# Performance work log

Hardware: AMD Instinct MI355X
Metric: run time of the kernel (lower is better)

## Reference

```python
import jax, jax.numpy as jnp
import numpy as np

B, S, D, H, DK, DFF = 4, 1024, 1024, 16, 64, 4096
EPS = 1e-5


def _layernorm(x, w, b):
    mu = jnp.mean(x, axis=-1, keepdims=True)
    var = jnp.mean((x - mu) ** 2, axis=-1, keepdims=True)
    return (x - mu) / jnp.sqrt(var + EPS) * w + b


def setup_inputs() -> dict:
    root = jax.random.key(0)
    ks = jax.random.split(root, 16)
    g = lambda k, shape, s=0.02: (jax.random.normal(k, shape, dtype=jnp.float32) * s)
    return {
        "mask": 1,
        "query": jax.random.normal(ks[0], (B, S, D), dtype=jnp.float32),
        "key": jax.random.normal(ks[1], (B, S, D), dtype=jnp.float32),
        "values": jax.random.normal(ks[2], (B, S, D), dtype=jnp.float32),
        "Wq": g(ks[3], (D, D)), "bq": jnp.zeros((D,), jnp.float32),
        "Wk": g(ks[4], (D, D)), "bk": jnp.zeros((D,), jnp.float32),
        "Wv": g(ks[5], (D, D)), "bv": jnp.zeros((D,), jnp.float32),
        "Wo": g(ks[6], (D, D)), "bo": jnp.zeros((D,), jnp.float32),
        "gammas": g(ks[7], (H, 1, 1), 0.5),
        "ln1_w": jnp.ones((D,), jnp.float32), "ln1_b": jnp.zeros((D,), jnp.float32),
        "W1": g(ks[8], (DFF, D)), "b1": jnp.zeros((DFF,), jnp.float32),
        "W2": g(ks[9], (D, DFF)), "b2": jnp.zeros((D,), jnp.float32),
        "ln2_w": jnp.ones((D,), jnp.float32), "ln2_b": jnp.zeros((D,), jnp.float32),
    }


def _forward(mask, query, key, values, Wq, bq, Wk, bk, Wv, bv, Wo, bo, gammas,
             ln1_w, ln1_b, W1, b1, W2, b2, ln2_w, ln2_b):
    # mask is a static Python int (the triu offset)
    allowed = jnp.triu(jnp.ones((S, S), dtype=jnp.float32), k=mask) == 0  # [S,S] bool

    def proj(x, W, b):  # [B,S,D] -> [B,H,S,DK]
        return (x @ W.T + b).reshape(B, S, H, DK).transpose(0, 2, 1, 3)

    q = proj(query, Wq, bq)
    k = proj(key, Wk, bk)
    v = proj(values, Wv, bv)

    scores = jnp.einsum('bhid,bhjd->bhij', q, k) / jnp.sqrt(jnp.float32(DK))

    # distance-decay factor, computed without gradient (torch.no_grad + detach)
    def dist_block(sc):
        sc_ = jax.nn.softmax(sc, axis=-1) * allowed.astype(sc.dtype)
        distcum = jnp.cumsum(sc_, axis=-1)
        disttot = jnp.sum(sc_, axis=-1, keepdims=True)
        idx = jnp.arange(S, dtype=jnp.float32)
        pos = jnp.abs(idx[None, :] - idx[:, None])[None, None]  # [1,1,S,S]
        return jnp.sqrt(jnp.clip((disttot - distcum) * pos, 0.0, None))
    dist_scores = jax.lax.stop_gradient(dist_block(scores))

    gamma = -jax.nn.softplus(gammas)[None]  # [1,H,1,1]
    total_effect = jnp.clip(jnp.exp(dist_scores * gamma), 1e-5, 1e5)
    scores = scores * total_effect
    scores = jnp.where(allowed, scores, jnp.float32(-1e20))
    attn = jax.nn.softmax(scores, axis=-1)
    if mask == 0:  # zero_pad first query row
        attn = attn.at[:, :, 0, :].set(0.0)

    out = jnp.einsum('bhij,bhjd->bhid', attn, v)
    concat = out.transpose(0, 2, 1, 3).reshape(B, S, D)
    attn_out = concat @ Wo.T + bo

    x = _layernorm(query + attn_out, ln1_w, ln1_b)
    ffn = jax.nn.relu(x @ W1.T + b1) @ W2.T + b2
    return _layernorm(x + ffn, ln2_w, ln2_b)


def reference(mask, query, key, values, Wq, bq, Wk, bk, Wv, bv, Wo, bo, gammas,
              ln1_w, ln1_b, W1, b1, W2, b2, ln2_w, ln2_b):
    return _forward(mask, query, key, values, Wq, bq, Wk, bk, Wv, bv, Wo, bo,
                    gammas, ln1_w, ln1_b, W1, b1, W2, b2, ln2_w, ln2_b)
```

## Files before the change

### kernel.cpp

```cpp
#include <hip/hip_runtime.h>
#include <hip/hip_bf16.h>
#include <math.h>

#define BB   4
#define SS   1024
#define DDIM 1024
#define HH   16
#define DKK  64
#define DFFF 4096
#define JC2  64

typedef __attribute__((ext_vector_type(8))) short short8;
typedef __attribute__((ext_vector_type(4))) float f32x4;
typedef unsigned short ushort;

__device__ __forceinline__ ushort f2bf(float f) {
    unsigned int u = __float_as_uint(f);
    unsigned int r = (u + 0x7FFFu + ((u >> 16) & 1u)) >> 16;
    return (ushort)r;
}
__device__ __forceinline__ short8 pack8(float4 f0, float4 f1) {
    short8 s;
    s[0] = (short)f2bf(f0.x); s[1] = (short)f2bf(f0.y);
    s[2] = (short)f2bf(f0.z); s[3] = (short)f2bf(f0.w);
    s[4] = (short)f2bf(f1.x); s[5] = (short)f2bf(f1.y);
    s[6] = (short)f2bf(f1.z); s[7] = (short)f2bf(f1.w);
    return s;
}

#define GLD16(g, l) __builtin_amdgcn_global_load_lds( \
    (const __attribute__((address_space(1))) unsigned int*)(g), \
    (__attribute__((address_space(3))) unsigned int*)(l), 16, 0, 0)

__device__ __forceinline__ float fexp2(float x) { return __builtin_amdgcn_exp2f(x); }

__device__ __forceinline__ float scan16(float x) {
    x += __int_as_float(__builtin_amdgcn_update_dpp(0, __float_as_int(x), 0x111, 0xF, 0xF, true));
    x += __int_as_float(__builtin_amdgcn_update_dpp(0, __float_as_int(x), 0x112, 0xF, 0xF, true));
    x += __int_as_float(__builtin_amdgcn_update_dpp(0, __float_as_int(x), 0x114, 0xF, 0xF, true));
    x += __int_as_float(__builtin_amdgcn_update_dpp(0, __float_as_int(x), 0x118, 0xF, 0xF, true));
    return x;
}
__device__ __forceinline__ float bcast15(float x) {
    return __int_as_float(__builtin_amdgcn_ds_swizzle(__float_as_int(x), 0x1F0));
}

__device__ __forceinline__ float block_reduce_sum(float v, float* red, int tid) {
#pragma unroll
    for (int off = 32; off; off >>= 1) v += __shfl_xor(v, off);
    __syncthreads();
    if ((tid & 63) == 0) red[tid >> 6] = v;
    __syncthreads();
    return red[0] + red[1] + red[2] + red[3];
}

struct CvtArgs { const float* s[9]; ushort* d[9]; unsigned int n[9]; };
__global__ __launch_bounds__(256) void convert_bf(CvtArgs a) {
    const int seg = blockIdx.y;
    size_t idx = ((size_t)blockIdx.x * 256 + threadIdx.x) * 8;
    if (idx >= a.n[seg]) return;
    const float* s = a.s[seg];
    float4 f0 = *(const float4*)(s + idx);
    float4 f1 = *(const float4*)(s + idx + 4);
    *(short8*)(a.d[seg] + idx) = pack8(f0, f1);
}

template <int BM, typename TC, bool RELU>
__device__ __forceinline__ void gemm_core(const ushort* __restrict__ A,
                                          const ushort* __restrict__ Bm,
                                          const float* __restrict__ bias,
                                          TC* __restrict__ C,
                                          int M, int N, int K,
                                          int bm, int bn) {
    constexpr int MT = BM / 32;
    constexpr int PA = BM / 32;
    __shared__ ushort A_s[BM * 64];
    __shared__ ushort B_s[128 * 64];
    const int t = threadIdx.x;
    const int lane = t & 63, w = t >> 6;
    const int wr = w >> 1, wc = w & 1;
    const int fm = lane & 15, fq = lane >> 4;
    const int srl = lane >> 3;
    const int sg8 = ((lane & 7) ^ srl) << 3;

    f32x4 acc[MT][4];
#pragma unroll
    for (int mt = 0; mt < MT; mt++)
#pragma unroll
        for (int nt = 0; nt < 4; nt++) acc[mt][nt] = (f32x4){0.f, 0.f, 0.f, 0.f};

    for (int kt = 0; kt < K; kt += 64) {
        __syncthreads();
#pragma unroll
        for (int p = 0; p < PA; ++p) {
            int rowg = (w * PA + p) * 8;
            GLD16(A + (size_t)(bm + rowg + srl) * K + kt + sg8, &A_s[rowg * 64]);
        }
#pragma unroll
        for (int p = 0; p < 4; ++p) {
            int rowg = (w * 4 + p) * 8;
            GLD16(Bm + (size_t)(bn + rowg + srl) * K + kt + sg8, &B_s[rowg * 64]);
        }
        __syncthreads();

        short8 av[2][MT], bv[2][4];
        const int sw = fm & 7;
#pragma unroll
        for (int mt = 0; mt < MT; ++mt) {
            int row = wr * (BM / 2) + mt * 16 + fm;
#pragma unroll
            for (int ks = 0; ks < 2; ++ks)
                av[ks][mt] = *(const short8*)&A_s[row * 64 + (((ks * 4 + fq) ^ sw) << 3)];
        }
#pragma unroll
        for (int nt = 0; nt < 4; ++nt) {
            int row = wc * 64 + nt * 16 + fm;
#pragma unroll
            for (int ks = 0; ks < 2; ++ks)
                bv[ks][nt] = *(const short8*)&B_s[row * 64 + (((ks * 4 + fq) ^ sw) << 3)];
        }
#pragma unroll
        for (int ks = 0; ks < 2; ++ks)
#pragma unroll
            for (int mt = 0; mt < MT; ++mt)
#pragma unroll
                for (int nt = 0; nt < 4; ++nt)
                    acc[mt][nt] = __builtin_amdgcn_mfma_f32_16x16x32_bf16(
                        av[ks][mt], bv[ks][nt], acc[mt][nt], 0, 0, 0);
    }

#pragma unroll
    for (int mt = 0; mt < MT; mt++) {
        int row0 = bm + wr * (BM / 2) + mt * 16 + fq * 4;
#pragma unroll
        for (int nt = 0; nt < 4; nt++) {
            int col = bn + wc * 64 + nt * 16 + fm;
            float bsv = bias[col];
#pragma unroll
            for (int r = 0; r < 4; r++) {
                float val = acc[mt][nt][r] + bsv;
                if (RELU) val = fmaxf(val, 0.f);
                if constexpr (sizeof(TC) == 4)
                    ((float*)C)[(size_t)(row0 + r) * N + col] = val;
                else
                    ((ushort*)C)[(size_t)(row0 + r) * N + col] = f2bf(val);
            }
        }
    }
}

template <int BM, typename TC, bool RELU>
__global__ __launch_bounds__(256, 2) void gemm_bf(const ushort* __restrict__ A,
                                                  const ushort* __restrict__ Bm,
                                                  const float* __restrict__ bias,
                                                  TC* __restrict__ C,
                                                  int M, int N, int K) {
    gemm_core<BM, TC, RELU>(A, Bm, bias, C, M, N, K,
                            blockIdx.y * BM, blockIdx.x * 128);
}

struct QkvArgs { const ushort* A[3]; const ushort* B[3]; const float* bias[3]; ushort* C[3]; };
__global__ __launch_bounds__(256, 2) void gemm_qkv(QkvArgs qa) {
    const int g = blockIdx.z;
    gemm_core<128, ushort, false>(qa.A[g], qa.B[g], qa.bias[g], qa.C[g],
                                  BB * SS, DDIM, DDIM,
                                  blockIdx.y * 128, blockIdx.x * 128);
}

__global__ __launch_bounds__(256, 4) void attn_flash(
    const ushort* __restrict__ Q, const ushort* __restrict__ Kg,
    const ushort* __restrict__ Vg, const float* __restrict__ gammas,
    const int* __restrict__ maskp, ushort* __restrict__ out) {
    __shared__ short QP[64 * 72];
    __shared__ short Ks[JC2 * 72];
    __shared__ short Vts[64 * 72];

    const int t = threadIdx.x;
    const int lane = t & 63, w = t >> 6;
    const int col = lane & 15;
    const int quad = lane >> 4;

    const int bid = blockIdx.x;
    const int it = bid >> 6;
    const int bh = bid & 63;
    const int h = bh & (HH - 1);
    const int b = bh >> 4;
    const int i0 = it * 64;
    const int mask = *maskp;

    const float LOG2E = 1.44269504f;
    const float SC2 = 0.125f * LOG2E;
    const float g0 = gammas[h];
    const float gnat = -((g0 > 20.f) ? g0 : log1pf(__expf(g0)));
    const float g2 = gnat * LOG2E;

    const size_t qbase = ((size_t)(b * SS + i0)) * DDIM + h * DKK;
    const size_t kvbase = ((size_t)b * SS) * DDIM + h * DKK;

    {
        int r = t >> 2, d0 = (t & 3) << 4;
        const ushort* gq = Q + qbase + (size_t)r * DDIM + d0;
        *(short8*)&QP[r * 72 + d0]     = *(const short8*)(gq);
        *(short8*)&QP[r * 72 + d0 + 8] = *(const short8*)(gq + 8);
    }
    __syncthreads();
    const short8 qa0 = *(const short8*)&QP[(w * 16 + col) * 72 + quad * 8];
    const short8 qa1 = *(const short8*)&QP[(w * 16 + col) * 72 + 32 + quad * 8];

    float m1[4], su[4], smT[4], gi4[4];
    int lim4[4];
#pragma unroll
    for (int r = 0; r < 4; ++r) {
        m1[r] = -3.4e38f; su[r] = 0.f; smT[r] = 0.f;
        int gi = i0 + w * 16 + quad * 4 + r;
        gi4[r] = (float)gi;
        lim4[r] = gi + mask;
    }

    for (int ck = 0; ck < SS / JC2; ++ck) {
        const int jc = ck * JC2;
        __syncthreads();
        {
            int j = t >> 2, d0 = (t & 3) << 4;
            const ushort* gk = Kg + kvbase + (size_t)(jc + j) * DDIM + d0;
            *(short8*)&Ks[j * 72 + d0]     = *(const short8*)(gk);
            *(short8*)&Ks[j * 72 + d0 + 8] = *(const short8*)(gk + 8);
        }
        __syncthreads();
#pragma unroll
        for (int g = 0; g < 4; ++g) {
            short8 kb0 = *(const short8*)&Ks[(g * 16 + col) * 72 + quad * 8];
            short8 kb1 = *(const short8*)&Ks[(g * 16 + col) * 72 + 32 + quad * 8];
            f32x4 c = (f32x4){0.f, 0.f, 0.f, 0.f};
            c = __builtin_amdgcn_mfma_f32_16x16x32_bf16(qa0, kb0, c, 0, 0, 0);
            c = __builtin_amdgcn_mfma_f32_16x16x32_bf16(qa1, kb1, c, 0, 0, 0);
            int j = jc + g * 16 + col;
#pragma unroll
            for (int r = 0; r < 4; ++r) {
                float s2 = c[r] * SC2;
                m1[r] = fmaxf(m1[r], s2);
                float ev = fexp2(s2);
                su[r] += ev;
                smT[r] += (j < lim4[r]) ? ev : 0.f;
            }
        }
    }
#pragma unroll
    for (int off = 1; off < 16; off <<= 1) {
#pragma unroll
        for (int r = 0; r < 4; ++r) {
            m1[r] = fmaxf(m1[r], __shfl_xor(m1[r], off, 16));
            su[r] += __shfl_xor(su[r], off, 16);
            smT[r] += __shfl_xor(smT[r], off, 16);
        }
    }
    float lse2[4], smTn[4], ms2[4];
#pragma unroll
    for (int r = 0; r < 4; ++r) {
        lse2[r] = __log2f(su[r]);
        smTn[r] = smT[r] / su[r];
        ms2[r]  = fmaxf(m1[r], 0.f);
    }

    const int nck2 = min(SS / JC2, max(1, (i0 + 62 + mask) / 64 + 1));

    float l2[4], carry[4];
    f32x4 o[4];
#pragma unroll
    for (int r = 0; r < 4; ++r) { l2[r] = 0.f; carry[r] = 0.f; }
#pragma unroll
    for (int dg = 0; dg < 4; ++dg) o[dg] = (f32x4){0.f, 0.f, 0.f, 0.f};

    short* Pw = &QP[w * 16 * 72];

    for (int ck = 0; ck < nck2; ++ck) {
        const int jc = ck * JC2;
        __syncthreads();
        {
            int j = t >> 2, d0 = (t & 3) << 4;
            const ushort* gk = Kg + kvbase + (size_t)(jc + j) * DDIM + d0;
            *(short8*)&Ks[j * 72 + d0]     = *(const short8*)(gk);
            *(short8*)&Ks[j * 72 + d0 + 8] = *(const short8*)(gk + 8);
        }
        {
            int j = t & 63, dq = t >> 6, d0 = dq * 16;
            const ushort* gv = Vg + kvbase + (size_t)(jc + j) * DDIM + d0;
            short8 v0 = *(const short8*)(gv);
            short8 v1 = *(const short8*)(gv + 8);
#pragma unroll
            for (int k = 0; k < 8; ++k) {
                Vts[(d0 + k) * 72 + j]     = v0[k];
                Vts[(d0 + 8 + k) * 72 + j] = v1[k];
            }
        }
        __syncthreads();

#pragma unroll
        for (int g = 0; g < 4; ++g) {
            short8 kb0 = *(const short8*)&Ks[(g * 16 + col) * 72 + quad * 8];
            short8 kb1 = *(const short8*)&Ks[(g * 16 + col) * 72 + 32 + quad * 8];
            f32x4 c = (f32x4){0.f, 0.f, 0.f, 0.f};
            c = __builtin_amdgcn_mfma_f32_16x16x32_bf16(qa0, kb0, c, 0, 0, 0);
            c = __builtin_amdgcn_mfma_f32_16x16x32_bf16(qa1, kb1, c, 0, 0, 0);
            const int j = jc + g * 16 + col;
            const float jf = (float)j;
#pragma unroll
            for (int r = 0; r < 4; ++r) {
                float s2 = c[r] * SC2;
                float pj = fexp2(s2 - lse2[r]);
                float incl = (j < lim4[r]) ? pj : 0.f;
                incl = scan16(incl);
                float tot = bcast15(incl);
                float Cc = carry[r] + incl;
                carry[r] += tot;
                float pos = fabsf(jf - gi4[r]);
                float d2 = fmaxf((smTn[r] - Cc) * pos, 0.f);
                float dist = __builtin_amdgcn_sqrtf(d2);
                float eff = fmaxf(fexp2(g2 * dist), 1e-5f);
                float pe = fexp2(s2 * eff - ms2[r]);
                float p = (j < lim4[r]) ? pe : 0.f;
                l2[r] += p;
                Pw[(quad * 4 + r) * 72 + g * 16 + col] = (short)f2bf(p);
            }
        }
        __syncthreads();
#pragma unroll
        for (int kg = 0; kg < 2; ++kg) {
            short8 pa = *(const short8*)&Pw[col * 72 + kg * 32 + quad * 8];
#pragma unroll
            for (int dg = 0; dg < 4; ++dg) {
                short8 vb = *(const short8*)&Vts[(dg * 16 + col) * 72 + kg * 32 + quad * 8];
                o[dg] = __builtin_amdgcn_mfma_f32_16x16x32_bf16(pa, vb, o[dg], 0, 0, 0);
            }
        }
    }

#pragma unroll
    for (int off = 1; off < 16; off <<= 1)
#pragma unroll
        for (int r = 0; r < 4; ++r) l2[r] += __shfl_xor(l2[r], off, 16);

#pragma unroll
    for (int r = 0; r < 4; ++r) {
        int irow = i0 + w * 16 + quad * 4 + r;
        float scl = 1.f / l2[r];
        if (mask == 0 && irow == 0) scl = 0.f;
        size_t base = ((size_t)(b * SS) + irow) * DDIM + h * DKK;
#pragma unroll
        for (int dg = 0; dg < 4; ++dg)
            out[base + dg * 16 + col] = f2bf(o[dg][r] * scl);
    }
}

template <bool WB>
__global__ __launch_bounds__(256) void add_ln(const float* __restrict__ R,
                                              const float* __restrict__ Y,
                                              const float* __restrict__ w,
                                              const float* __restrict__ bb,
                                              float* __restrict__ out,
                                              ushort* __restrict__ obf) {
    const int row = blockIdx.x;
    const int tid = threadIdx.x;
    __shared__ float red[4];
    __shared__ float xs[DDIM];
    const size_t base = (size_t)row * DDIM;
    float s = 0.f, s2 = 0.f;
#pragma unroll
    for (int l = 0; l < 4; l++) {
        int idx = tid + l * 256;
        float x = R[base + idx] + Y[base + idx];
        xs[idx] = x;
        s += x;
        s2 += x * x;
    }
    s = block_reduce_sum(s, red, tid);
    s2 = block_reduce_sum(s2, red, tid);
    const float mu = s * (1.f / DDIM);
    const float var = s2 * (1.f / DDIM) - mu * mu;
    const float rstd = rsqrtf(var + 1e-5f);
#pragma unroll
    for (int l = 0; l < 4; l++) {
        int idx = tid + l * 256;
        float v = (xs[idx] - mu) * rstd * w[idx] + bb[idx];
        out[base + idx] = v;
        if (WB) obf[base + idx] = f2bf(v);
    }
}

extern "C" void kernel_launch(void* const* d_in, const int* in_sizes, int n_in,
                              void* d_out, int out_size, void* d_ws, size_t ws_size,
                              hipStream_t stream) {
    const int*   maskp  = (const int*)d_in[0];
    const float* query  = (const float*)d_in[1];
    const float* key    = (const float*)d_in[2];
    const float* values = (const float*)d_in[3];
    const float* Wq = (const float*)d_in[4];
    const float* bq = (const float*)d_in[5];
    const float* Wk = (const float*)d_in[6];
    const float* bk = (const float*)d_in[7];
    const float* Wv = (const float*)d_in[8];
    const float* bv = (const float*)d_in[9];
    const float* Wo = (const float*)d_in[10];
    const float* bo = (const float*)d_in[11];
    const float* gammas = (const float*)d_in[12];
    const float* ln1w = (const float*)d_in[13];
    const float* ln1b = (const float*)d_in[14];
    const float* W1 = (const float*)d_in[15];
    const float* b1 = (const float*)d_in[16];
    const float* W2 = (const float*)d_in[17];
    const float* b2 = (const float*)d_in[18];
    const float* ln2w = (const float*)d_in[19];
    const float* ln2b = (const float*)d_in[20];

    const int M = BB * SS;
    const size_t MB = 1048576;
    char* wsb = (char*)d_ws;
    ushort* Wq_bf = (ushort*)(wsb + 0 * MB);
    ushort* Wk_bf = (ushort*)(wsb + 8 * MB);
    ushort* Wv_bf = (ushort*)(wsb + 16 * MB);
    ushort* Wo_bf = (ushort*)(wsb + 24 * MB);
    ushort* W1_bf = (ushort*)(wsb + 32 * MB);
    ushort* W2_bf = (ushort*)(wsb + 40 * MB);
    ushort* qi_bf = (ushort*)(wsb + 48 * MB);
    ushort* ki_bf = (ushort*)(wsb + 56 * MB);
    ushort* vi_bf = (ushort*)(wsb + 64 * MB);
    ushort* Qb    = (ushort*)(wsb + 72 * MB);
    ushort* Kb    = (ushort*)(wsb + 80 * MB);
    ushort* Vb    = (ushort*)(wsb + 88 * MB);
    ushort* ATTb  = (ushort*)(wsb + 96 * MB);
    float*  Yf    = (float*)(wsb + 104 * MB);
    float*  xf    = (float*)(wsb + 48 * MB);
    ushort* x_bf  = (ushort*)(wsb + 64 * MB);
    ushort* hidden= (ushort*)(wsb + 72 * MB);

    dim3 blk(256);

    const unsigned int N4M = 4u * 1024 * 1024, N1M = 1024 * 1024;
    CvtArgs ca;
    ca.s[0] = query; ca.s[1] = key; ca.s[2] = values;
    ca.s[3] = Wq; ca.s[4] = Wk; ca.s[5] = Wv; ca.s[6] = Wo;
    ca.s[7] = W1; ca.s[8] = W2;
    ca.d[0] = qi_bf; ca.d[1] = ki_bf; ca.d[2] = vi_bf;
    ca.d[3] = Wq_bf; ca.d[4] = Wk_bf; ca.d[5] = Wv_bf; ca.d[6] = Wo_bf;
    ca.d[7] = W1_bf; ca.d[8] = W2_bf;
    ca.n[0] = N4M; ca.n[1] = N4M; ca.n[2] = N4M;
    ca.n[3] = N1M; ca.n[4] = N1M; ca.n[5] = N1M; ca.n[6] = N1M;
    ca.n[7] = N4M; ca.n[8] = N4M;
    convert_bf<<<dim3(2048, 9), blk, 0, stream>>>(ca);

    QkvArgs qa;
    qa.A[0] = qi_bf; qa.A[1] = ki_bf; qa.A[2] = vi_bf;
    qa.B[0] = Wq_bf; qa.B[1] = Wk_bf; qa.B[2] = Wv_bf;
    qa.bias[0] = bq; qa.bias[1] = bk; qa.bias[2] = bv;
    qa.C[0] = Qb; qa.C[1] = Kb; qa.C[2] = Vb;
    gemm_qkv<<<dim3(8, 32, 3), blk, 0, stream>>>(qa);

    attn_flash<<<dim3(BB * HH * 16), blk, 0, stream>>>(Qb, Kb, Vb, gammas, maskp, ATTb);

    gemm_bf<64, float, false><<<dim3(8, 64), blk, 0, stream>>>(ATTb, Wo_bf, bo, Yf, M, DDIM, DDIM);

    add_ln<true><<<dim3(M), blk, 0, stream>>>(query, Yf, ln1w, ln1b, xf, x_bf);

    gemm_bf<128, ushort, true><<<dim3(32, 32), blk, 0, stream>>>(x_bf, W1_bf, b1, hidden, M, DFFF, DDIM);

    gemm_bf<64, float, false><<<dim3(8, 64), blk, 0, stream>>>(hidden, W2_bf, b2, Yf, M, DDIM, DFFF);

    add_ln<false><<<dim3(M), blk, 0, stream>>>(xf, Yf, ln2w, ln2b, (float*)d_out, nullptr);
}
```

Baseline: 418.0 us.

## Split-K the output and FFN2 GEMMs with 128-row tiles, reduce in LayerNorm

```diff
diff --git a/kernel.cpp b/kernel.cpp
--- a/kernel.cpp
+++ b/kernel.cpp
@@ -65,12 +65,11 @@
     *(short8*)(a.d[seg] + idx) = pack8(f0, f1);
 }
 
-template <int BM, typename TC, bool RELU>
-__device__ __forceinline__ void gemm_core(const ushort* __restrict__ A,
-                                          const ushort* __restrict__ Bm,
+template <int BM, typename TC, bool RELU, bool BIAS>
+__device__ __forceinline__ void gemm_core(const ushort* __restrict__ A, int lda,
+                                          const ushort* __restrict__ Bm, int ldb,
                                           const float* __restrict__ bias,
-                                          TC* __restrict__ C,
-                                          int M, int N, int K,
+                                          TC* __restrict__ C, int N, int Klen,
                                           int bm, int bn) {
     constexpr int MT = BM / 32;
     constexpr int PA = BM / 32;
@@ -89,17 +88,17 @@
 #pragma unroll
         for (int nt = 0; nt < 4; nt++) acc[mt][nt] = (f32x4){0.f, 0.f, 0.f, 0.f};
 
-    for (int kt = 0; kt < K; kt += 64) {
+    for (int kt = 0; kt < Klen; kt += 64) {
         __syncthreads();
 #pragma unroll
         for (int p = 0; p < PA; ++p) {
             int rowg = (w * PA + p) * 8;
-            GLD16(A + (size_t)(bm + rowg + srl) * K + kt + sg8, &A_s[rowg * 64]);
+            GLD16(A + (size_t)(bm + rowg + srl) * lda + kt + sg8, &A_s[rowg * 64]);
         }
 #pragma unroll
         for (int p = 0; p < 4; ++p) {
             int rowg = (w * 4 + p) * 8;
-            GLD16(Bm + (size_t)(bn + rowg + srl) * K + kt + sg8, &B_s[rowg * 64]);
+            GLD16(Bm + (size_t)(bn + rowg + srl) * ldb + kt + sg8, &B_s[rowg * 64]);
         }
         __syncthreads();
 
@@ -135,7 +134,7 @@
 #pragma unroll
         for (int nt = 0; nt < 4; nt++) {
             int col = bn + wc * 64 + nt * 16 + fm;
-            float bsv = bias[col];
+            float bsv = BIAS ? bias[col] : 0.f;
 #pragma unroll
             for (int r = 0; r < 4; r++) {
                 float val = acc[mt][nt][r] + bsv;
@@ -154,17 +153,27 @@
                                                   const ushort* __restrict__ Bm,
                                                   const float* __restrict__ bias,
                                                   TC* __restrict__ C,
-                                                  int M, int N, int K) {
-    gemm_core<BM, TC, RELU>(A, Bm, bias, C, M, N, K,
-                            blockIdx.y * BM, blockIdx.x * 128);
+                                                  int N, int K) {
+    gemm_core<BM, TC, RELU, true>(A, K, Bm, K, bias, C, N, K,
+                                  blockIdx.y * BM, blockIdx.x * 128);
 }
 
 struct QkvArgs { const ushort* A[3]; const ushort* B[3]; const float* bias[3]; ushort* C[3]; };
 __global__ __launch_bounds__(256, 2) void gemm_qkv(QkvArgs qa) {
     const int g = blockIdx.z;
-    gemm_core<128, ushort, false>(qa.A[g], qa.B[g], qa.bias[g], qa.C[g],
-                                  BB * SS, DDIM, DDIM,
-                                  blockIdx.y * 128, blockIdx.x * 128);
+    gemm_core<128, ushort, false, true>(qa.A[g], DDIM, qa.B[g], DDIM,
+                                        qa.bias[g], qa.C[g], DDIM, DDIM,
+                                        blockIdx.y * 128, blockIdx.x * 128);
+}
+
+struct SkArgs { const ushort* A; const ushort* Bm; float* C0; float* C1; int lda; int Klen; };
+__global__ __launch_bounds__(256, 2) void gemm_splitk(SkArgs s) {
+    const int z = blockIdx.z;
+    float* C = z ? s.C1 : s.C0;
+    const int koff = z * s.Klen;
+    gemm_core<128, float, false, false>(s.A + koff, s.lda, s.Bm + koff, s.lda,
+                                        nullptr, C, DDIM, s.Klen,
+                                        blockIdx.y * 128, blockIdx.x * 128);
 }
 
 __global__ __launch_bounds__(256, 4) void attn_flash(
@@ -354,7 +363,9 @@
 
 template <bool WB>
 __global__ __launch_bounds__(256) void add_ln(const float* __restrict__ R,
-                                              const float* __restrict__ Y,
+                                              const float* __restrict__ Y0,
+                                              const float* __restrict__ Y1,
+                                              const float* __restrict__ gb,
                                               const float* __restrict__ w,
                                               const float* __restrict__ bb,
                                               float* __restrict__ out,
@@ -368,7 +379,7 @@
 #pragma unroll
     for (int l = 0; l < 4; l++) {
         int idx = tid + l * 256;
-        float x = R[base + idx] + Y[base + idx];
+        float x = R[base + idx] + Y0[base + idx] + Y1[base + idx] + gb[idx];
         xs[idx] = x;
         s += x;
         s2 += x * x;
@@ -428,7 +439,8 @@
     ushort* Kb    = (ushort*)(wsb + 80 * MB);
     ushort* Vb    = (ushort*)(wsb + 88 * MB);
     ushort* ATTb  = (ushort*)(wsb + 96 * MB);
-    float*  Yf    = (float*)(wsb + 104 * MB);
+    float*  Ysp0  = (float*)(wsb + 104 * MB);
+    float*  Ysp1  = (float*)(wsb + 0 * MB);
     float*  xf    = (float*)(wsb + 48 * MB);
     ushort* x_bf  = (ushort*)(wsb + 64 * MB);
     ushort* hidden= (ushort*)(wsb + 72 * MB);
@@ -457,13 +469,21 @@
 
     attn_flash<<<dim3(BB * HH * 16), blk, 0, stream>>>(Qb, Kb, Vb, gammas, maskp, ATTb);
 
-    gemm_bf<64, float, false><<<dim3(8, 64), blk, 0, stream>>>(ATTb, Wo_bf, bo, Yf, M, DDIM, DDIM);
-
-    add_ln<true><<<dim3(M), blk, 0, stream>>>(query, Yf, ln1w, ln1b, xf, x_bf);
-
-    gemm_bf<128, ushort, true><<<dim3(32, 32), blk, 0, stream>>>(x_bf, W1_bf, b1, hidden, M, DFFF, DDIM);
-
-    gemm_bf<64, float, false><<<dim3(8, 64), blk, 0, stream>>>(hidden, W2_bf, b2, Yf, M, DDIM, DFFF);
-
-    add_ln<false><<<dim3(M), blk, 0, stream>>>(xf, Yf, ln2w, ln2b, (float*)d_out, nullptr);
-}
+    {
+        SkArgs s; s.A = ATTb; s.Bm = Wo_bf; s.C0 = Ysp0; s.C1 = Ysp1;
+        s.lda = DDIM; s.Klen = DDIM / 2;
+        gemm_splitk<<<dim3(8, 32, 2), blk, 0, stream>>>(s);
+    }
+
+    add_ln<true><<<dim3(M), blk, 0, stream>>>(query, Ysp0, Ysp1, bo, ln1w, ln1b, xf, x_bf);
+
+    gemm_bf<128, ushort, true><<<dim3(32, 32), blk, 0, stream>>>(x_bf, W1_bf, b1, hidden, DFFF, DDIM);
+
+    {
+        SkArgs s; s.A = hidden; s.Bm = W2_bf; s.C0 = Ysp0; s.C1 = Ysp1;
+        s.lda = DFFF; s.Klen = DFFF / 2;
+        gemm_splitk<<<dim3(8, 32, 2), blk, 0, stream>>>(s);
+    }
+
+    add_ln<false><<<dim3(M), blk, 0, stream>>>(xf, Ysp0, Ysp1, b2, ln2w, ln2b, (float*)d_out, nullptr);
+}
```

New measurement: 411.1 us. No clear change (-1.7%).
